# Kernel tuning notes

Measured on AMD Instinct MI355X. Metric: run time of the kernel, lower is better.

Reference implementation:

```python
import jax, jax.numpy as jnp
import numpy as np

T, B, E, H, R, NHASH, CHUNK = 2048, 2, 1024, 8, 2, 8, 32
D = E // H
INF = 1.0e16  # module's self.inf
BIG = 1.0e8   # module's self.big


def setup_inputs() -> dict:
    key = jax.random.key(0)
    ks = jax.random.split(key, 8)
    w = lambda k, shape, s=0.02: jax.random.normal(k, shape, dtype=jnp.float32) * s
    return {
        "query": jax.random.normal(ks[0], (T, B, E), jnp.float32),
        "key":   jax.random.normal(ks[1], (T, B, E), jnp.float32),
        "value": jax.random.normal(ks[2], (T, B, E), jnp.float32),
        "Wq": w(ks[3], (E, E)), "bq": jnp.zeros((E,), jnp.float32),
        "Wv": w(ks[4], (E, E)), "bv": jnp.zeros((E,), jnp.float32),
        "Wo": w(ks[5], (E, E)), "bo": jnp.zeros((E,), jnp.float32),
        "hash_w": w(ks[6], (R, H, D, NHASH // 2), 0.1),
    }


def _hashes(x_tbhd, hash_w):
    # einsum('ibnf,rnfh->ibrnh'), cat([lin,-lin]), argmax -> [T,B,R,H]
    lin = jnp.einsum('tbhd,rhdn->tbrhn', x_tbhd, hash_w)
    return jnp.argmax(jnp.concatenate([lin, -lin], axis=-1), axis=-1)


def _gather_t(x_bhtd, perm_brht):
    # gather along T with per-(b,r,h) permutation -> [B,R,H,T,D]
    Bb, Rr, Hh, Tt = perm_brht.shape
    Dd = x_bhtd.shape[-1]
    xb = jnp.broadcast_to(x_bhtd[:, None], (Bb, Rr, Hh, Tt, Dd))
    idx = jnp.broadcast_to(perm_brht[..., None], (Bb, Rr, Hh, Tt, Dd))
    return jnp.take_along_axis(xb, idx, axis=3)


def reference(query, key, value, Wq, bq, Wv, bv, Wo, bo, hash_w):
    del key  # share_kq=True (self-attention): keys are L2-normalized queries
    scaling = D ** -0.5
    qf = query @ Wq + bq                                    # [T,B,E]
    kf = qf / jnp.linalg.norm(qf, axis=-1, keepdims=True)   # F.normalize over embed dim
    vf = value @ Wv + bv
    q = qf.reshape(T, B, H, D) * scaling
    k = kf.reshape(T, B, H, D)
    v = vf.reshape(T, B, H, D)

    q_hash = _hashes(q, hash_w)                             # [T,B,R,H]
    k_hash = _hashes(k, hash_w)

    qh_t = jnp.transpose(q_hash, (1, 2, 3, 0))              # [B,R,H,T]
    kh_t = jnp.transpose(k_hash, (1, 2, 3, 0))
    p_q = jnp.argsort(qh_t, axis=-1)                        # stable sort by hash
    p_k = jnp.argsort(kh_t, axis=-1)
    inv_q = jnp.argsort(p_q, axis=-1)                       # sorted position of each token

    q_s = _gather_t(jnp.transpose(q, (1, 2, 0, 3)), p_q)    # [B,R,H,T,D]
    k_s = _gather_t(jnp.transpose(k, (1, 2, 0, 3)), p_k)
    v_s = _gather_t(jnp.transpose(v, (1, 2, 0, 3)), p_k)
    qh_s = jnp.take_along_axis(qh_t, p_q, axis=-1)
    kh_s = jnp.take_along_axis(kh_t, p_k, axis=-1)

    C = T // CHUNK
    M = 3 * CHUNK
    chunk = lambda x: x.reshape(x.shape[:3] + (C, CHUNK) + x.shape[4:])
    q_c, qh_c, qid_c = chunk(q_s), chunk(qh_s), chunk(p_q)
    k_c, v_c, kh_c, kid_c = chunk(k_s), chunk(v_s), chunk(kh_s), chunk(p_k)

    # each query chunk attends key chunks {c-1, c, c+1} (num_chunk_offsets=3, wraparound)
    blocks = lambda x: jnp.concatenate([jnp.roll(x, 1, axis=3), x, jnp.roll(x, -1, axis=3)], axis=4)
    kb, vb, khb, kidb = blocks(k_c), blocks(v_c), blocks(kh_c), blocks(kid_c)

    scores = jnp.einsum('brhcld,brhcmd->brhclm', q_c, kb)   # q pre-scaled by d^-0.5
    scores = scores - INF * (qh_c[..., :, None] != khb[..., None, :])   # mask_different_hashes
    scores = scores - BIG * (qid_c[..., :, None] == kidb[..., None, :]) # mask_current

    # cross-round duplicate counting: key ids attended per original query
    chunk_of = inv_q // CHUNK                               # [B,R,H,T]
    idx = jnp.broadcast_to(chunk_of[..., None], (B, R, H, T, M))
    A = jnp.take_along_axis(kidb, idx, axis=3)              # [B,R,H,T,M]
    dup = []
    for r in range(R):
        c = jnp.zeros((B, H, T, M), jnp.int32)
        for r2 in range(R):
            c = c + (A[:, r, :, :, :, None] == A[:, r2, :, :, None, :]).sum(-1, dtype=jnp.int32)
        dup.append(c)
    dup = jnp.stack(dup, axis=1)                            # [B,R,H,T,M]
    idx2 = jnp.broadcast_to(p_q[..., None], (B, R, H, T, M))
    dup_s = jnp.take_along_axis(dup, idx2, axis=3)          # sorted-query order
    scores = scores - jnp.log(dup_s.astype(scores.dtype)).reshape(scores.shape)

    z = jax.nn.logsumexp(scores, axis=-1)                   # [B,R,H,C,L]
    attn = jax.nn.softmax(scores, axis=-1)
    o = jnp.einsum('brhclm,brhcmd->brhcld', attn, vb).reshape(B, R, H, T, D)
    z = z.reshape(B, R, H, T)

    # scatter back to original token order
    idx3 = jnp.broadcast_to(inv_q[..., None], (B, R, H, T, D))
    o = jnp.take_along_axis(o, idx3, axis=3)
    z = jnp.take_along_axis(z, inv_q, axis=3)

    w = jax.nn.softmax(z, axis=1)                           # combine rounds by logsumexp weight
    out = (w[..., None] * o).sum(axis=1)                    # [B,H,T,D]
    out = jnp.transpose(out, (2, 0, 1, 3)).reshape(T, B, E)
    return out @ Wo + bo
```

## Files before the change

kernel.cpp:

```cpp
#include <hip/hip_runtime.h>

typedef unsigned short ushort_t;
typedef __bf16 bf16x8 __attribute__((ext_vector_type(8)));
typedef float f32x4 __attribute__((ext_vector_type(4)));

#define T_DIM 2048
#define B_DIM 2
#define E_DIM 1024
#define H_DIM 8
#define R_DIM 2
#define D_DIM 128
#define M_WIN 96
#define SCALING 0.08838834764831845f
#define LN2F 0.69314718055994530942f

__device__ __forceinline__ float bfu(unsigned u) {
  union { unsigned i; float f; } x; x.i = u << 16; return x.f;
}
__device__ __forceinline__ unsigned f2bf(float f) {
  union { float f; unsigned i; } x; x.f = f;
  unsigned r = x.i + 0x7fffu + ((x.i >> 16) & 1u);
  return r >> 16;
}
__device__ __forceinline__ void gl_lds16(const void* g, void* l) {
  __builtin_amdgcn_global_load_lds(
      (const __attribute__((address_space(1))) unsigned int*)g,
      (__attribute__((address_space(3))) unsigned int*)l, 16, 0, 0);
}

__global__ __launch_bounds__(256) void prep_kernel(
    const float* __restrict__ query, const float* __restrict__ value,
    const float* __restrict__ Wq, const float* __restrict__ Wv,
    const float* __restrict__ Wo, const float* __restrict__ bq,
    const float* __restrict__ hw,
    ushort_t* __restrict__ qh, ushort_t* __restrict__ vh,
    ushort_t* __restrict__ WqT, ushort_t* __restrict__ WvT,
    ushort_t* __restrict__ WoT, float* __restrict__ F, float* __restrict__ cvec)
{
  __shared__ float plds[4160];
  const int bid = blockIdx.x, tid = threadIdx.x;
  if (bid < 8192) {
    const float* src = (bid < 4096) ? query : value;
    ushort_t* dst = (bid < 4096) ? qh : vh;
    int i = ((bid & 4095) * 256 + tid) * 4;
    float4 x = *(const float4*)&src[i];
    uint2 oh;
    oh.x = f2bf(x.x) | (f2bf(x.y) << 16);
    oh.y = f2bf(x.z) | (f2bf(x.w) << 16);
    *(uint2*)&dst[i] = oh;
  } else if (bid < 8960) {
    int idx = bid - 8192;
    const float* in = (idx < 256) ? Wq : (idx < 512) ? Wv : Wo;
    ushort_t* hi = (idx < 256) ? WqT : (idx < 512) ? WvT : WoT;
    int tile = idx & 255;
    int n0 = (tile & 15) * 64, k0 = (tile >> 4) * 64;
    float (*t64)[65] = (float(*)[65])plds;
    const int tr = tid >> 4, tc4 = (tid & 15) * 4;
#pragma unroll
    for (int rr = 0; rr < 64; rr += 16)
      *(float4*)&t64[tr + rr][tc4] = *(const float4*)&in[(size_t)(k0 + tr + rr) * E_DIM + n0 + tc4];
    __syncthreads();
#pragma unroll
    for (int rr = 0; rr < 64; rr += 16) {
      int n = n0 + tr + rr;
      uint2 oh;
      oh.x = f2bf(t64[tc4 + 0][tr + rr]) | (f2bf(t64[tc4 + 1][tr + rr]) << 16);
      oh.y = f2bf(t64[tc4 + 2][tr + rr]) | (f2bf(t64[tc4 + 3][tr + rr]) << 16);
      *(uint2*)&hi[(size_t)n * E_DIM + k0 + tc4] = oh;
    }
  } else {
    float* wl = plds;
    const int rh = bid - 8960, h = rh & 7;
    for (int i = tid; i < 512; i += 256) wl[i] = hw[rh * 512 + i];
    __syncthreads();
    for (int e = tid; e < E_DIM; e += 256) {
      const float* wr = Wq + (size_t)e * E_DIM + h * D_DIM;
      float a0 = 0.f, a1 = 0.f, a2 = 0.f, a3 = 0.f;
      for (int d = 0; d < 128; d += 4) {
        float4 q4 = *(const float4*)&wr[d];
        float4 w0 = *(const float4*)&wl[d * 4];
        float4 w1 = *(const float4*)&wl[d * 4 + 4];
        float4 w2 = *(const float4*)&wl[d * 4 + 8];
        float4 w3 = *(const float4*)&wl[d * 4 + 12];
        a0 += q4.x * w0.x + q4.y * w1.x + q4.z * w2.x + q4.w * w3.x;
        a1 += q4.x * w0.y + q4.y * w1.y + q4.z * w2.y + q4.w * w3.y;
        a2 += q4.x * w0.z + q4.y * w1.z + q4.z * w2.z + q4.w * w3.z;
        a3 += q4.x * w0.w + q4.y * w1.w + q4.z * w2.w + q4.w * w3.w;
      }
      float4 o; o.x = a0; o.y = a1; o.z = a2; o.w = a3;
      *(float4*)&F[(size_t)e * 64 + rh * 4] = o;
    }
    if (tid < 4) {
      float acc = 0.f;
      for (int d = 0; d < 128; ++d) acc += bq[h * D_DIM + d] * wl[d * 4 + tid];
      cvec[rh * 4 + tid] = acc;
    }
  }
}

__global__ __launch_bounds__(256) void hashlin_kernel(const float* __restrict__ query,
                                                      const float* __restrict__ F,
                                                      const float* __restrict__ cvec,
                                                      int* __restrict__ hashb)
{
  __shared__ float As[32][17];
  __shared__ float Fs[32][64];
  const int tid = threadIdx.x;
  const int ty = tid >> 4, tx = tid & 15;
  const int r0 = blockIdx.x * 16;
  float acc0 = 0.f, acc1 = 0.f, acc2 = 0.f, acc3 = 0.f;
  for (int k0 = 0; k0 < E_DIM; k0 += 32) {
    __syncthreads();
    {
      int i = tid * 2, row = i >> 5, kk = i & 31;
      float2 a2 = *(const float2*)&query[(size_t)(r0 + row) * E_DIM + k0 + kk];
      As[kk][row] = a2.x; As[kk + 1][row] = a2.y;
    }
    {
      int i = tid * 8, kk = i >> 6, cc = i & 63;
      float4 f0 = *(const float4*)&F[(size_t)(k0 + kk) * 64 + cc];
      float4 f1 = *(const float4*)&F[(size_t)(k0 + kk) * 64 + cc + 4];
      *(float4*)&Fs[kk][cc] = f0;
      *(float4*)&Fs[kk][cc + 4] = f1;
    }
    __syncthreads();
#pragma unroll
    for (int kk = 0; kk < 32; ++kk) {
      float a = As[kk][ty];
      float4 f4 = *(const float4*)&Fs[kk][tx * 4];
      acc0 += a * f4.x; acc1 += a * f4.y; acc2 += a * f4.z; acc3 += a * f4.w;
    }
  }
  float4 c4 = *(const float4*)&cvec[tx * 4];
  float lin[4] = {acc0 + c4.x, acc1 + c4.y, acc2 + c4.z, acc3 + c4.w};
  float best = lin[0]; int bi = 0;
#pragma unroll
  for (int idx = 1; idx < 8; ++idx) {
    float v = (idx < 4) ? lin[idx] : -lin[idx - 4];
    if (v > best) { best = v; bi = idx; }
  }
  int grow = r0 + ty;
  int t = grow >> 1, b = grow & 1;
  int rr = tx >> 3, hh = tx & 7;
  hashb[(size_t)((b * R_DIM + rr) * H_DIM + hh) * T_DIM + t] = bi;
}

__global__ __launch_bounds__(256) void gemm_mfma(
    const ushort_t* __restrict__ A0, const ushort_t* __restrict__ B0,
    const float* __restrict__ bias0, ushort_t* __restrict__ Cb0, float* __restrict__ Cf0,
    const ushort_t* __restrict__ A1, const ushort_t* __restrict__ B1,
    const float* __restrict__ bias1, ushort_t* __restrict__ Cb1, float* __restrict__ Cf1)
{
  const ushort_t* Ah = blockIdx.z ? A1 : A0;
  const ushort_t* Bh = blockIdx.z ? B1 : B0;
  const float* bias = blockIdx.z ? bias1 : bias0;
  ushort_t* Cb = blockIdx.z ? Cb1 : Cb0;
  float* Cf = blockIdx.z ? Cf1 : Cf0;

  __shared__ ushort_t As[128 * 32];
  __shared__ ushort_t Bs[128 * 32];
  const int tid = threadIdx.x, w = tid >> 6, lane = tid & 63;
  const int lm = lane & 15, quad = lane >> 4;
  const int wr = w >> 1, wc = w & 1;
  const int m0 = blockIdx.y * 128, n0 = blockIdx.x * 128;
  const int lrow = lane >> 2, lcol = (lane & 3) * 8;

  f32x4 acc[4][4] = {};

  for (int k0 = 0; k0 < E_DIM; k0 += 32) {
    __syncthreads();
#pragma unroll
    for (int k = 0; k < 8; ++k) {
      if ((k & 3) == w) {
        gl_lds16(Ah + (size_t)(m0 + k * 16 + lrow) * E_DIM + k0 + lcol, &As[k * 512]);
        gl_lds16(Bh + (size_t)(n0 + k * 16 + lrow) * E_DIM + k0 + lcol, &Bs[k * 512]);
      }
    }
    __syncthreads();
    bf16x8 av[4], bv[4];
#pragma unroll
    for (int i = 0; i < 4; ++i) av[i] = *(const bf16x8*)&As[(wr * 64 + i * 16 + lm) * 32 + quad * 8];
#pragma unroll
    for (int j = 0; j < 4; ++j) bv[j] = *(const bf16x8*)&Bs[(wc * 64 + j * 16 + lm) * 32 + quad * 8];
#pragma unroll
    for (int i = 0; i < 4; ++i)
#pragma unroll
      for (int j = 0; j < 4; ++j)
        acc[i][j] = __builtin_amdgcn_mfma_f32_16x16x32_bf16(av[i], bv[j], acc[i][j], 0, 0, 0);
  }
#pragma unroll
  for (int j = 0; j < 4; ++j) {
    int col = n0 + wc * 64 + j * 16 + lm;
    float bj = bias[col];
#pragma unroll
    for (int i = 0; i < 4; ++i) {
      int rowb = m0 + wr * 64 + i * 16 + quad * 4;
#pragma unroll
      for (int rg = 0; rg < 4; ++rg) {
        float val = acc[i][j][rg] + bj;
        if (Cb) Cb[(size_t)(rowb + rg) * E_DIM + col] = (ushort_t)f2bf(val);
        else    Cf[(size_t)(rowb + rg) * E_DIM + col] = val;
      }
    }
  }
}

__global__ __launch_bounds__(256) void normsort_kernel(
    const ushort_t* __restrict__ qfb, float* __restrict__ inv_nrm,
    const int* __restrict__ hashb, int* __restrict__ p, int* __restrict__ inv)
{
  __shared__ int mat[8][256];
  __shared__ int btot[8], bbase[8];
  __shared__ float part[4];
  const int tid = threadIdx.x;
  if (blockIdx.x < 4096) {
    int row = blockIdx.x;
    uint2 u = *(const uint2*)&qfb[((size_t)row << 10) + tid * 4];
    float a0 = bfu(u.x & 0xffffu), a1 = bfu(u.x >> 16);
    float a2 = bfu(u.y & 0xffffu), a3 = bfu(u.y >> 16);
    float s = a0 * a0 + a1 * a1 + a2 * a2 + a3 * a3;
    for (int off = 1; off < 64; off <<= 1) s += __shfl_xor(s, off);
    if ((tid & 63) == 0) part[tid >> 6] = s;
    __syncthreads();
    if (tid == 0) {
      float t = part[0] + part[1] + part[2] + part[3];
      inv_nrm[row] = 1.0f / sqrtf(t);
    }
    return;
  }
  const int bid = blockIdx.x - 4096;
  const int lane = tid & 63, w = tid >> 6;
  const int* hrow = hashb + (size_t)bid * T_DIM;
  int cnt[8];
#pragma unroll
  for (int v = 0; v < 8; ++v) cnt[v] = 0;
  int hv[8];
#pragma unroll
  for (int j = 0; j < 8; ++j) { hv[j] = hrow[tid * 8 + j]; cnt[hv[j]]++; }
#pragma unroll
  for (int v = 0; v < 8; ++v) mat[v][tid] = cnt[v];
  __syncthreads();
  for (int v = w; v < 8; v += 4) {
    int4 c4 = *(const int4*)&mat[v][lane * 4];
    int s = c4.x + c4.y + c4.z + c4.w;
    int x = s;
    for (int off = 1; off < 64; off <<= 1) {
      int y = __shfl_up(x, off);
      if (lane >= off) x += y;
    }
    int excl = x - s;
    mat[v][lane * 4 + 0] = excl;
    mat[v][lane * 4 + 1] = excl + c4.x;
    mat[v][lane * 4 + 2] = excl + c4.x + c4.y;
    mat[v][lane * 4 + 3] = excl + c4.x + c4.y + c4.z;
    if (lane == 63) btot[v] = x;
  }
  __syncthreads();
  if (tid == 0) {
    int run = 0;
    for (int v = 0; v < 8; ++v) { bbase[v] = run; run += btot[v]; }
  }
  __syncthreads();
#pragma unroll
  for (int v = 0; v < 8; ++v) cnt[v] = 0;
#pragma unroll
  for (int j = 0; j < 8; ++j) {
    int v = hv[j];
    int pos = bbase[v] + mat[v][tid] + cnt[v];
    cnt[v]++;
    p[(size_t)bid * T_DIM + pos] = tid * 8 + j;
    inv[(size_t)bid * T_DIM + tid * 8 + j] = pos;
  }
}

__global__ __launch_bounds__(256) void gather_kernel(
    const ushort_t* __restrict__ qfb, const ushort_t* __restrict__ vfb,
    const float* __restrict__ inv_nrm, const int* __restrict__ hashb,
    const int* __restrict__ p, const int* __restrict__ inv,
    int* __restrict__ meta_s, float* __restrict__ invn_s,
    ushort_t* __restrict__ ksort, ushort_t* __restrict__ vt)
{
  const int c = blockIdx.x, brh = blockIdx.y;
  const int b = brh >> 4, h = brh & 7;
  const int brh_o = brh ^ 8;
  const int tid = threadIdx.x;
  __shared__ int ts[32];
  __shared__ ushort_t vtile[32 * 136];

  if (tid < 32) {
    int pos = c * 32 + tid;
    int t = p[(size_t)brh * T_DIM + pos];
    int hh = hashb[(size_t)brh * T_DIM + t];
    int co = inv[(size_t)brh_o * T_DIM + t] >> 5;
    meta_s[(size_t)brh * T_DIM + pos] = t | (hh << 11) | (co << 14);
    invn_s[(size_t)brh * T_DIM + pos] = inv_nrm[t * B_DIM + b];
    ts[tid] = t;
  }
  __syncthreads();
  {
    int i = tid >> 3, part = tid & 7;
    int t = ts[i];
    const ushort_t* src = qfb + ((size_t)(t * B_DIM + b) << 10) + h * D_DIM + part * 16;
    uint4 a = *(const uint4*)src;
    uint4 bb = *(const uint4*)(src + 8);
    ushort_t* dst = ksort + ((size_t)brh * T_DIM + c * 32 + i) * 136 + part * 16;
    *(uint4*)dst = a; *(uint4*)(dst + 8) = bb;
    const ushort_t* vsrc = vfb + ((size_t)(t * B_DIM + b) << 10) + h * D_DIM + part * 16;
    uint4 va = *(const uint4*)vsrc;
    uint4 vb = *(const uint4*)(vsrc + 8);
    ushort_t* vdst = &vtile[i * 136 + part * 16];
    *(uint4*)vdst = va; *(uint4*)(vdst + 8) = vb;
  }
  __syncthreads();
  {
    int d = tid >> 1, half = tid & 1;
    unsigned pk[8];
#pragma unroll
    for (int jj = 0; jj < 8; ++jj) {
      unsigned lo = vtile[(half * 16 + jj * 2) * 136 + d];
      unsigned hi = vtile[(half * 16 + jj * 2 + 1) * 136 + d];
      pk[jj] = lo | (hi << 16);
    }
    ushort_t* out = vt + ((size_t)(brh * 64 + c)) * 4096 + d * 32 + half * 16;
    uint4 o0; o0.x = pk[0]; o0.y = pk[1]; o0.z = pk[2]; o0.w = pk[3];
    uint4 o1; o1.x = pk[4]; o1.y = pk[5]; o1.z = pk[6]; o1.w = pk[7];
    *(uint4*)out = o0; *(uint4*)(out + 8) = o1;
  }
}

__global__ __launch_bounds__(256) void attn_kernel(
    const ushort_t* __restrict__ ksort, const ushort_t* __restrict__ vt,
    const int* __restrict__ meta_s, const float* __restrict__ invn_s,
    ushort_t* __restrict__ o_out, float* __restrict__ z_out)
{
  const int c = blockIdx.x, h = blockIdx.y, bz = blockIdx.z;
  const int b = bz >> 1, r = bz & 1;
  const int brh = (b * R_DIM + r) * H_DIM + h;
  const int tid = threadIdx.x;
  const int lane = tid & 63, w = tid >> 6;
  const int lm = lane & 15, quad = lane >> 4;

  __shared__ __align__(16) unsigned char smem[50688];
  ushort_t* Kw = (ushort_t*)smem;
  ushort_t* VTb = (ushort_t*)(smem + 26112);
  float*    SS = (float*)smem;
  ushort_t* Ps = (ushort_t*)(smem + 13312);
  __shared__ int skp[M_WIN];
  __shared__ float s_invn[M_WIN];

  int cjs[3] = {(c + 63) & 63, c, (c + 1) & 63};

  int cnt = 0;
#pragma unroll
  for (int j = 0; j < 3; ++j) {
    const ushort_t* gk = ksort + ((size_t)brh * T_DIM + cjs[j] * 32) * 136;
    ushort_t* lk = Kw + j * 4352;
#pragma unroll
    for (int k = 0; k < 8; ++k) {
      if ((cnt++ & 3) == w) gl_lds16(gk + k * 512 + lane * 8, lk + k * 512);
    }
    if ((cnt++ & 3) == w) {
      if (lane < 32) gl_lds16(gk + 4096 + lane * 8, lk + 4096);
    }
  }
#pragma unroll
  for (int j = 0; j < 3; ++j) {
    const ushort_t* gv = vt + ((size_t)(brh * 64 + cjs[j])) * 4096;
    ushort_t* lv = VTb + j * 4096;
#pragma unroll
    for (int k = 0; k < 8; ++k) {
      if ((cnt++ & 3) == w) gl_lds16(gv + k * 512 + lane * 8, lv + k * 512);
    }
  }
  if (tid < M_WIN) {
    int pos = cjs[tid >> 5] * 32 + (tid & 31);
    skp[tid] = meta_s[(size_t)brh * T_DIM + pos];
    s_invn[tid] = invn_s[(size_t)brh * T_DIM + pos];
  }
  __syncthreads();

  const int mw = w & 1, nset = w >> 1;
  bf16x8 av[4];
#pragma unroll
  for (int kk = 0; kk < 4; ++kk)
    av[kk] = *(const bf16x8*)&Kw[(32 + mw * 16 + lm) * 136 + kk * 32 + quad * 8];
  f32x4 sacc[3] = {};
#pragma unroll
  for (int jj = 0; jj < 3; ++jj) {
    int nt = nset * 3 + jj;
#pragma unroll
    for (int kk = 0; kk < 4; ++kk) {
      bf16x8 bv = *(const bf16x8*)&Kw[(nt * 16 + lm) * 136 + kk * 32 + quad * 8];
      sacc[jj] = __builtin_amdgcn_mfma_f32_16x16x32_bf16(av[kk], bv, sacc[jj], 0, 0, 0);
    }
  }
  __syncthreads();

  const int rowb = mw * 16 + quad * 4;
#pragma unroll
  for (int jj = 0; jj < 3; ++jj) {
    int col = (nset * 3 + jj) * 16 + lm;
    int kp = skp[col];
    float scl = SCALING * s_invn[col];
#pragma unroll
    for (int rg = 0; rg < 4; ++rg) {
      int qp = skp[32 + rowb + rg];
      float sc = sacc[jj][rg] * scl;
      if ((kp ^ qp) & 0x3800) sc -= 1.0e16f;
      if (!((kp ^ qp) & 0x7FF)) sc -= 1.0e8f;
      int dc = ((kp >> 14) - (qp >> 14)) & 63;
      if (dc <= 1 || dc == 63) sc -= LN2F;
      SS[(rowb + rg) * 100 + col] = sc;
    }
  }
  __syncthreads();

  {
    const int l = tid >> 3, g = tid & 7;
    float smy[12];
#pragma unroll
    for (int j = 0; j < 12; ++j) smy[j] = SS[l * 100 + g + 8 * j];
    float mx = smy[0];
#pragma unroll
    for (int j = 1; j < 12; ++j) mx = fmaxf(mx, smy[j]);
    mx = fmaxf(mx, __shfl_xor(mx, 1));
    mx = fmaxf(mx, __shfl_xor(mx, 2));
    mx = fmaxf(mx, __shfl_xor(mx, 4));
    float sum = 0.f, ey[12];
#pragma unroll
    for (int j = 0; j < 12; ++j) { ey[j] = expf(smy[j] - mx); sum += ey[j]; }
    sum += __shfl_xor(sum, 1);
    sum += __shfl_xor(sum, 2);
    sum += __shfl_xor(sum, 4);
    float inv_s = 1.0f / sum;
#pragma unroll
    for (int j = 0; j < 12; ++j)
      Ps[l * 104 + g + 8 * j] = (ushort_t)f2bf(ey[j] * inv_s);
    if (g == 0) z_out[(size_t)brh * T_DIM + (skp[32 + l] & 2047)] = mx + logf(sum);
  }
  __syncthreads();

  const int dset = w >> 1;
  bf16x8 pa[3];
#pragma unroll
  for (int kk = 0; kk < 3; ++kk)
    pa[kk] = *(const bf16x8*)&Ps[(mw * 16 + lm) * 104 + kk * 32 + quad * 8];
  f32x4 oacc[4] = {};
#pragma unroll
  for (int jj = 0; jj < 4; ++jj) {
    int dt = dset * 4 + jj;
#pragma unroll
    for (int kk = 0; kk < 3; ++kk) {
      const ushort_t* VTk = VTb + kk * 4096;
      bf16x8 bv = *(const bf16x8*)&VTk[(dt * 16 + lm) * 32 + quad * 8];
      oacc[jj] = __builtin_amdgcn_mfma_f32_16x16x32_bf16(pa[kk], bv, oacc[jj], 0, 0, 0);
    }
  }
#pragma unroll
  for (int jj = 0; jj < 4; ++jj) {
    int col = (dset * 4 + jj) * 16 + lm;
#pragma unroll
    for (int rg = 0; rg < 4; ++rg) {
      int tqo = skp[32 + rowb + rg] & 2047;
      o_out[((size_t)brh * T_DIM + tqo) * D_DIM + col] = (ushort_t)f2bf(oacc[jj][rg]);
    }
  }
}

__global__ __launch_bounds__(256) void combine_kernel(const ushort_t* __restrict__ obf,
                                                      const float* __restrict__ z_buf,
                                                      ushort_t* __restrict__ ctx)
{
  int gid = blockIdx.x * 256 + threadIdx.x;
  int d4 = gid & 31;
  int t = (gid >> 5) & (T_DIM - 1);
  int h = (gid >> 16) & 7;
  int b = gid >> 19;
  int brh0 = (b * R_DIM + 0) * H_DIM + h;
  int brh1 = brh0 + H_DIM;
  float z0 = z_buf[(size_t)brh0 * T_DIM + t], z1 = z_buf[(size_t)brh1 * T_DIM + t];
  float mz = fmaxf(z0, z1);
  float e0 = expf(z0 - mz), e1 = expf(z1 - mz);
  float is = 1.0f / (e0 + e1);
  float w0 = e0 * is, w1 = e1 * is;
  uint2 a = *(const uint2*)&obf[((size_t)brh0 * T_DIM + t) * D_DIM + d4 * 4];
  uint2 cc = *(const uint2*)&obf[((size_t)brh1 * T_DIM + t) * D_DIM + d4 * 4];
  uint2 o;
  o.x = f2bf(w0 * bfu(a.x & 0xffffu) + w1 * bfu(cc.x & 0xffffu)) |
        (f2bf(w0 * bfu(a.x >> 16) + w1 * bfu(cc.x >> 16)) << 16);
  o.y = f2bf(w0 * bfu(a.y & 0xffffu) + w1 * bfu(cc.y & 0xffffu)) |
        (f2bf(w0 * bfu(a.y >> 16) + w1 * bfu(cc.y >> 16)) << 16);
  *(uint2*)&ctx[((size_t)(t * B_DIM + b) << 10) + h * D_DIM + d4 * 4] = o;
}

extern "C" void kernel_launch(void* const* d_in, const int* in_sizes, int n_in,
                              void* d_out, int out_size, void* d_ws, size_t ws_size,
                              hipStream_t stream)
{
  const float* query = (const float*)d_in[0];
  const float* value = (const float*)d_in[2];
  const float* Wq = (const float*)d_in[3];
  const float* bq = (const float*)d_in[4];
  const float* Wv = (const float*)d_in[5];
  const float* bv = (const float*)d_in[6];
  const float* Wo = (const float*)d_in[7];
  const float* bo = (const float*)d_in[8];
  const float* hw = (const float*)d_in[9];

  float* ws = (float*)d_ws;
  ushort_t* qh    = (ushort_t*)ws;
  ushort_t* vh    = qh + 4194304;
  ushort_t* obuf  = qh;
  ushort_t* qfb   = (ushort_t*)(ws + 4194304);
  ushort_t* ctx   = qfb;
  ushort_t* vfb   = qfb + 4194304;
  ushort_t* ksort = vfb + 4194304;
  ushort_t* vt    = ksort + 8912896;
  ushort_t* WqTh  = vt + 8388608;
  ushort_t* WvTh  = WqTh + 1048576;
  ushort_t* WoTh  = WvTh + 1048576;
  float* F        = (float*)(WoTh + 1048576);
  float* cvec     = F + 65536;
  float* zbuf     = cvec + 64;
  float* inv_nrm  = zbuf + 65536;
  int* hashb      = (int*)(inv_nrm + 4096);
  int* pperm      = hashb + 65536;
  int* pinv       = pperm + 65536;
  int* meta_s     = pinv + 65536;
  float* invn_s   = (float*)(meta_s + 65536);

  prep_kernel<<<8976, 256, 0, stream>>>(query, value, Wq, Wv, Wo, bq, hw,
                                        qh, vh, WqTh, WvTh, WoTh, F, cvec);
  hashlin_kernel<<<256, 256, 0, stream>>>(query, F, cvec, hashb);
  gemm_mfma<<<dim3(8, 32, 2), 256, 0, stream>>>(qh, WqTh, bq, qfb, (float*)nullptr,
                                                vh, WvTh, bv, vfb, (float*)nullptr);
  normsort_kernel<<<4128, 256, 0, stream>>>(qfb, inv_nrm, hashb, pperm, pinv);
  gather_kernel<<<dim3(64, 32), 256, 0, stream>>>(qfb, vfb, inv_nrm, hashb, pperm, pinv,
                                                  meta_s, invn_s, ksort, vt);
  attn_kernel<<<dim3(64, 8, 4), 256, 0, stream>>>(ksort, vt, meta_s, invn_s, obuf, zbuf);
  combine_kernel<<<4096, 256, 0, stream>>>(obuf, zbuf, ctx);
  gemm_mfma<<<dim3(8, 32, 1), 256, 0, stream>>>(ctx, WoTh, bo, (ushort_t*)nullptr, (float*)d_out,
                                                (const ushort_t*)nullptr, (const ushort_t*)nullptr,
                                                (const float*)nullptr, (ushort_t*)nullptr, (float*)nullptr);
}
```

Measured before the change: 283.1 us.

## Fuse query row-norm into Q projection GEMM epilogue and spread hash-weight prep

The L2 norm of each projected query row is now accumulated in the Q GEMM epilogue (from the bf16-rounded values) using wave shuffles and atomicAdd into a zeroed buffer. This removes the separate norm pass that re-read qfb inside the sort kernel, which now only sorts. The prep kernel also spreads the hash-projection precompute over 64 blocks instead of 16, and adds a block that zeroes the norm buffer. In exchange, atomics make the summation order nondeterministic, and the GEMM epilogue does extra work.

```diff
diff --git a/kernel.cpp b/kernel.cpp
--- a/kernel.cpp
+++ b/kernel.cpp
@@ -28,14 +28,15 @@
       (__attribute__((address_space(3))) unsigned int*)l, 16, 0, 0);
 }
 
-__global__ __launch_bounds__(256) void prep_kernel(
+__global__ __launch_bounds__(256, 4) void prep2_kernel(
     const float* __restrict__ query, const float* __restrict__ value,
     const float* __restrict__ Wq, const float* __restrict__ Wv,
     const float* __restrict__ Wo, const float* __restrict__ bq,
     const float* __restrict__ hw,
     ushort_t* __restrict__ qh, ushort_t* __restrict__ vh,
     ushort_t* __restrict__ WqT, ushort_t* __restrict__ WvT,
-    ushort_t* __restrict__ WoT, float* __restrict__ F, float* __restrict__ cvec)
+    ushort_t* __restrict__ WoT, float* __restrict__ F,
+    float* __restrict__ cvec, float* __restrict__ snorm)
 {
   __shared__ float plds[4160];
   const int bid = blockIdx.x, tid = threadIdx.x;
@@ -68,33 +69,37 @@
       oh.y = f2bf(t64[tc4 + 2][tr + rr]) | (f2bf(t64[tc4 + 3][tr + rr]) << 16);
       *(uint2*)&hi[(size_t)n * E_DIM + k0 + tc4] = oh;
     }
-  } else {
+  } else if (bid < 9024) {
     float* wl = plds;
-    const int rh = bid - 8960, h = rh & 7;
+    const int rh = (bid - 8960) & 15, h = rh & 7;
+    const int e = ((bid - 8960) >> 4) * 256 + tid;
     for (int i = tid; i < 512; i += 256) wl[i] = hw[rh * 512 + i];
     __syncthreads();
-    for (int e = tid; e < E_DIM; e += 256) {
-      const float* wr = Wq + (size_t)e * E_DIM + h * D_DIM;
-      float a0 = 0.f, a1 = 0.f, a2 = 0.f, a3 = 0.f;
-      for (int d = 0; d < 128; d += 4) {
-        float4 q4 = *(const float4*)&wr[d];
-        float4 w0 = *(const float4*)&wl[d * 4];
-        float4 w1 = *(const float4*)&wl[d * 4 + 4];
-        float4 w2 = *(const float4*)&wl[d * 4 + 8];
-        float4 w3 = *(const float4*)&wl[d * 4 + 12];
-        a0 += q4.x * w0.x + q4.y * w1.x + q4.z * w2.x + q4.w * w3.x;
-        a1 += q4.x * w0.y + q4.y * w1.y + q4.z * w2.y + q4.w * w3.y;
-        a2 += q4.x * w0.z + q4.y * w1.z + q4.z * w2.z + q4.w * w3.z;
-        a3 += q4.x * w0.w + q4.y * w1.w + q4.z * w2.w + q4.w * w3.w;
-      }
-      float4 o; o.x = a0; o.y = a1; o.z = a2; o.w = a3;
-      *(float4*)&F[(size_t)e * 64 + rh * 4] = o;
-    }
-    if (tid < 4) {
+    const float* wr = Wq + (size_t)e * E_DIM + h * D_DIM;
+    float a0 = 0.f, a1 = 0.f, a2 = 0.f, a3 = 0.f;
+#pragma unroll 2
+    for (int d = 0; d < 128; d += 2) {
+      float2 q2 = *(const float2*)&wr[d];
+      float4 w0 = *(const float4*)&wl[d * 4];
+      float4 w1 = *(const float4*)&wl[d * 4 + 4];
+      a0 += q2.x * w0.x + q2.y * w1.x;
+      a1 += q2.x * w0.y + q2.y * w1.y;
+      a2 += q2.x * w0.z + q2.y * w1.z;
+      a3 += q2.x * w0.w + q2.y * w1.w;
+    }
+    float4 o; o.x = a0; o.y = a1; o.z = a2; o.w = a3;
+    *(float4*)&F[(size_t)e * 64 + rh * 4] = o;
+    if ((bid - 8960) < 16 && tid < 4) {
       float acc = 0.f;
+#pragma unroll 1
       for (int d = 0; d < 128; ++d) acc += bq[h * D_DIM + d] * wl[d * 4 + tid];
       cvec[rh * 4 + tid] = acc;
     }
+  } else {
+    float4 z4 = {0.f, 0.f, 0.f, 0.f};
+#pragma unroll
+    for (int i = 0; i < 4; ++i)
+      *(float4*)&snorm[(i * 256 + tid) * 4] = z4;
   }
 }
 
@@ -149,7 +154,8 @@
     const ushort_t* __restrict__ A0, const ushort_t* __restrict__ B0,
     const float* __restrict__ bias0, ushort_t* __restrict__ Cb0, float* __restrict__ Cf0,
     const ushort_t* __restrict__ A1, const ushort_t* __restrict__ B1,
-    const float* __restrict__ bias1, ushort_t* __restrict__ Cb1, float* __restrict__ Cf1)
+    const float* __restrict__ bias1, ushort_t* __restrict__ Cb1, float* __restrict__ Cf1,
+    float* __restrict__ snorm, int do_norm)
 {
   const ushort_t* Ah = blockIdx.z ? A1 : A0;
   const ushort_t* Bh = blockIdx.z ? B1 : B0;
@@ -188,6 +194,8 @@
       for (int j = 0; j < 4; ++j)
         acc[i][j] = __builtin_amdgcn_mfma_f32_16x16x32_bf16(av[i], bv[j], acc[i][j], 0, 0, 0);
   }
+
+  float rs[4][4] = {};
 #pragma unroll
   for (int j = 0; j < 4; ++j) {
     int col = n0 + wc * 64 + j * 16 + lm;
@@ -198,39 +206,41 @@
 #pragma unroll
       for (int rg = 0; rg < 4; ++rg) {
         float val = acc[i][j][rg] + bj;
-        if (Cb) Cb[(size_t)(rowb + rg) * E_DIM + col] = (ushort_t)f2bf(val);
-        else    Cf[(size_t)(rowb + rg) * E_DIM + col] = val;
+        if (Cb) {
+          unsigned ub = f2bf(val);
+          Cb[(size_t)(rowb + rg) * E_DIM + col] = (ushort_t)ub;
+          float vb = bfu(ub);
+          rs[i][rg] += vb * vb;
+        } else {
+          Cf[(size_t)(rowb + rg) * E_DIM + col] = val;
+        }
       }
     }
   }
-}
-
-__global__ __launch_bounds__(256) void normsort_kernel(
-    const ushort_t* __restrict__ qfb, float* __restrict__ inv_nrm,
-    const int* __restrict__ hashb, int* __restrict__ p, int* __restrict__ inv)
-{
+  if (do_norm && blockIdx.z == 0) {
+#pragma unroll
+    for (int i = 0; i < 4; ++i)
+#pragma unroll
+      for (int rg = 0; rg < 4; ++rg) {
+        float s = rs[i][rg];
+        s += __shfl_xor(s, 1);
+        s += __shfl_xor(s, 2);
+        s += __shfl_xor(s, 4);
+        s += __shfl_xor(s, 8);
+        if (lm == 0)
+          atomicAdd(&snorm[m0 + wr * 64 + i * 16 + quad * 4 + rg], s);
+      }
+  }
+}
+
+__global__ __launch_bounds__(256) void sort_kernel(const int* __restrict__ hashb,
+                                                   int* __restrict__ p, int* __restrict__ inv)
+{
+  const int bid = blockIdx.x, tid = threadIdx.x;
+  const int lane = tid & 63, w = tid >> 6;
+  const int* hrow = hashb + (size_t)bid * T_DIM;
   __shared__ int mat[8][256];
   __shared__ int btot[8], bbase[8];
-  __shared__ float part[4];
-  const int tid = threadIdx.x;
-  if (blockIdx.x < 4096) {
-    int row = blockIdx.x;
-    uint2 u = *(const uint2*)&qfb[((size_t)row << 10) + tid * 4];
-    float a0 = bfu(u.x & 0xffffu), a1 = bfu(u.x >> 16);
-    float a2 = bfu(u.y & 0xffffu), a3 = bfu(u.y >> 16);
-    float s = a0 * a0 + a1 * a1 + a2 * a2 + a3 * a3;
-    for (int off = 1; off < 64; off <<= 1) s += __shfl_xor(s, off);
-    if ((tid & 63) == 0) part[tid >> 6] = s;
-    __syncthreads();
-    if (tid == 0) {
-      float t = part[0] + part[1] + part[2] + part[3];
-      inv_nrm[row] = 1.0f / sqrtf(t);
-    }
-    return;
-  }
-  const int bid = blockIdx.x - 4096;
-  const int lane = tid & 63, w = tid >> 6;
-  const int* hrow = hashb + (size_t)bid * T_DIM;
   int cnt[8];
 #pragma unroll
   for (int v = 0; v < 8; ++v) cnt[v] = 0;
@@ -275,7 +285,7 @@
 
 __global__ __launch_bounds__(256) void gather_kernel(
     const ushort_t* __restrict__ qfb, const ushort_t* __restrict__ vfb,
-    const float* __restrict__ inv_nrm, const int* __restrict__ hashb,
+    const float* __restrict__ snorm, const int* __restrict__ hashb,
     const int* __restrict__ p, const int* __restrict__ inv,
     int* __restrict__ meta_s, float* __restrict__ invn_s,
     ushort_t* __restrict__ ksort, ushort_t* __restrict__ vt)
@@ -293,7 +303,7 @@
     int hh = hashb[(size_t)brh * T_DIM + t];
     int co = inv[(size_t)brh_o * T_DIM + t] >> 5;
     meta_s[(size_t)brh * T_DIM + pos] = t | (hh << 11) | (co << 14);
-    invn_s[(size_t)brh * T_DIM + pos] = inv_nrm[t * B_DIM + b];
+    invn_s[(size_t)brh * T_DIM + pos] = 1.0f / sqrtf(snorm[t * B_DIM + b]);
     ts[tid] = t;
   }
   __syncthreads();
@@ -522,24 +532,26 @@
   float* F        = (float*)(WoTh + 1048576);
   float* cvec     = F + 65536;
   float* zbuf     = cvec + 64;
-  float* inv_nrm  = zbuf + 65536;
-  int* hashb      = (int*)(inv_nrm + 4096);
+  float* snorm    = zbuf + 65536;
+  int* hashb      = (int*)(snorm + 4096);
   int* pperm      = hashb + 65536;
   int* pinv       = pperm + 65536;
   int* meta_s     = pinv + 65536;
   float* invn_s   = (float*)(meta_s + 65536);
 
-  prep_kernel<<<8976, 256, 0, stream>>>(query, value, Wq, Wv, Wo, bq, hw,
-                                        qh, vh, WqTh, WvTh, WoTh, F, cvec);
+  prep2_kernel<<<9025, 256, 0, stream>>>(query, value, Wq, Wv, Wo, bq, hw,
+                                         qh, vh, WqTh, WvTh, WoTh, F, cvec, snorm);
   hashlin_kernel<<<256, 256, 0, stream>>>(query, F, cvec, hashb);
   gemm_mfma<<<dim3(8, 32, 2), 256, 0, stream>>>(qh, WqTh, bq, qfb, (float*)nullptr,
-                                                vh, WvTh, bv, vfb, (float*)nullptr);
-  normsort_kernel<<<4128, 256, 0, stream>>>(qfb, inv_nrm, hashb, pperm, pinv);
-  gather_kernel<<<dim3(64, 32), 256, 0, stream>>>(qfb, vfb, inv_nrm, hashb, pperm, pinv,
+                                                vh, WvTh, bv, vfb, (float*)nullptr,
+                                                snorm, 1);
+  sort_kernel<<<32, 256, 0, stream>>>(hashb, pperm, pinv);
+  gather_kernel<<<dim3(64, 32), 256, 0, stream>>>(qfb, vfb, snorm, hashb, pperm, pinv,
                                                   meta_s, invn_s, ksort, vt);
   attn_kernel<<<dim3(64, 8, 4), 256, 0, stream>>>(ksort, vt, meta_s, invn_s, obuf, zbuf);
   combine_kernel<<<4096, 256, 0, stream>>>(obuf, zbuf, ctx);
   gemm_mfma<<<dim3(8, 32, 1), 256, 0, stream>>>(ctx, WoTh, bo, (ushort_t*)nullptr, (float*)d_out,
                                                 (const ushort_t*)nullptr, (const ushort_t*)nullptr,
-                                                (const float*)nullptr, (ushort_t*)nullptr, (float*)nullptr);
-}
+                                                (const float*)nullptr, (ushort_t*)nullptr, (float*)nullptr,
+                                                snorm, 0);
+}
```

Measured after the change: 258.2 us. 1.1x faster.
